# Kernel optimization log

Measured on AMD Instinct MI355X. Metric: run time of the kernel, lower is better.

The kernel has to match this reference:

```python
import jax, jax.numpy as jnp
import numpy as np

B, C, H, W = 4, 256, 128, 128
OUT = 50

def setup_inputs() -> dict:
    key = jax.random.key(0)
    k1, k2, k3 = jax.random.split(key, 3)
    x = jax.random.normal(k1, (B, C, H, W), dtype=jnp.float32)
    # conv2d 1x1 weights, kaiming-ish scale
    W_f = jax.random.normal(k2, (OUT, C), dtype=jnp.float32) * (1.0 / np.sqrt(C))
    W_beta = jax.random.normal(k3, (C, C), dtype=jnp.float32) * (1.0 / np.sqrt(C))
    return {"x": x, "W_f": W_f, "W_beta": W_beta}

def reference(x, W_f, W_beta):
    b, c, h, w = x.shape
    n = h * w
    xf = x.reshape(b, c, n)                      # [B,C,N]
    F = jnp.einsum('oc,bcn->bon', W_f, xf)       # 1x1 conv -> [B,O,N]
    # S = softmax(F @ A, axis over C), A = xf^T : [B,N,C]
    S = jnp.einsum('bon,bcn->boc', F, xf)        # [B,O,C]
    S = jax.nn.softmax(S, axis=2)
    St = jnp.swapaxes(S, 1, 2)                   # [B,C,O]
    E = jnp.einsum('bco,bon->bcn', St, F)        # [B,C,N]
    E = E.reshape(b, c, h, w)
    E = jnp.einsum('dc,bchw->bdhw', W_beta, E) + x  # beta conv + residual
    return E
```

## Files before the change

kernel.cpp:

```cpp
#include <hip/hip_runtime.h>
#include <math.h>

#define CCH 256
#define OCH 50
#define NPIX 16384
#define BATCH 4
#define BO (BATCH*OCH)
#define NSPLIT2 256
#define KC2 (NPIX/NSPLIT2)

typedef _Float16 f16x8 __attribute__((ext_vector_type(8)));
typedef float f32x4 __attribute__((ext_vector_type(4)));
typedef unsigned int uint;
typedef unsigned short ushort;

__device__ __forceinline__ void cvt_split(const float4 v0, const float4 v1,
                                          f16x8& h, f16x8& l) {
    float v[8] = {v0.x, v0.y, v0.z, v0.w, v1.x, v1.y, v1.z, v1.w};
#pragma unroll
    for (int j = 0; j < 8; ++j) {
        _Float16 hj = (_Float16)v[j];
        h[j] = hj;
        l[j] = (_Float16)(v[j] - (float)hj);
    }
}

__device__ __forceinline__ uint packhl(float v) {
    _Float16 h = (_Float16)v;
    _Float16 l = (_Float16)(v - (float)h);
    union { _Float16 f; ushort u; } H, L;
    H.f = h; L.f = l;
    return (uint)H.u | ((uint)L.u << 16);
}

__device__ __forceinline__ void unpack8(const uint* w, f16x8& h, f16x8& l) {
    union { uint u[4]; f16x8 v; } H, L;
#pragma unroll
    for (int k = 0; k < 4; ++k) {
        H.u[k] = __builtin_amdgcn_perm(w[2 * k + 1], w[2 * k], 0x05040100u);
        L.u[k] = __builtin_amdgcn_perm(w[2 * k + 1], w[2 * k], 0x07060302u);
    }
    h = H.v; l = L.v;
}

__global__ void k0_pack(const float* __restrict__ Wf, uint* __restrict__ Wf16p) {
    int i = blockIdx.x * 256 + threadIdx.x;
    if (i < 64 * CCH) {
        int o = i / CCH;
        float v = (o < OCH) ? Wf[i] : 0.f;
        Wf16p[i] = packhl(v);
    }
}

__global__ __launch_bounds__(256, 4) void k12_mfma(const float* __restrict__ x,
                                                   const uint* __restrict__ Wf16p,
                                                   float* __restrict__ F,
                                                   float* __restrict__ Spart) {
    int b  = blockIdx.y;
    int ks = blockIdx.x;
    int p0 = ks * KC2;
    int t  = threadIdx.x;
    int w = t >> 6, lane = t & 63, r16 = lane & 15, kg = lane >> 4;
    __shared__ uint xl[2][32 * 64];
    __shared__ float Ft[4][16 * 68];

    int cidx = t & 15;
    int pixg = t >> 4;
    const float* xb = x + ((size_t)b * CCH) * NPIX + p0;

    float4 r0 = *(const float4*)(xb + (size_t)cidx * NPIX + pixg * 4);
    float4 r1 = *(const float4*)(xb + (size_t)(16 + cidx) * NPIX + pixg * 4);

    f32x4 acc[4];
#pragma unroll
    for (int nt = 0; nt < 4; ++nt) acc[nt] = {0.f, 0.f, 0.f, 0.f};

    const uint* Arow = Wf16p + (w * 16 + r16) * CCH;

    {
        float v0[4] = {r0.x, r0.y, r0.z, r0.w};
        float v1[4] = {r1.x, r1.y, r1.z, r1.w};
#pragma unroll
        for (int j = 0; j < 4; ++j) {
            int pix = pixg * 4 + j;
            int q = (pix & 7) << 2;
            xl[0][pix * 32 + (cidx ^ q)]        = packhl(v0[j]);
            xl[0][pix * 32 + ((16 + cidx) ^ q)] = packhl(v1[j]);
        }
    }
    __syncthreads();

#pragma unroll
    for (int s = 0; s < 8; ++s) {
        if (s < 7) {
            r0 = *(const float4*)(xb + (size_t)((s + 1) * 32 + cidx) * NPIX + pixg * 4);
            r1 = *(const float4*)(xb + (size_t)((s + 1) * 32 + 16 + cidx) * NPIX + pixg * 4);
        }
        uint aw[8];
        *(uint4*)aw       = *(const uint4*)(Arow + s * 32 + kg * 8);
        *(uint4*)(aw + 4) = *(const uint4*)(Arow + s * 32 + kg * 8 + 4);
        f16x8 Ah, Al;
        unpack8(aw, Ah, Al);

        const uint* buf = xl[s & 1];
#pragma unroll
        for (int nt = 0; nt < 4; ++nt) {
            int pix = nt * 16 + r16;
            int q = (r16 & 7) << 2;
            uint bw[8];
            *(uint4*)bw       = *(const uint4*)&buf[pix * 32 + ((kg * 8) ^ q)];
            *(uint4*)(bw + 4) = *(const uint4*)&buf[pix * 32 + ((kg * 8 + 4) ^ q)];
            f16x8 Bh, Bl;
            unpack8(bw, Bh, Bl);
            acc[nt] = __builtin_amdgcn_mfma_f32_16x16x32_f16(Ah, Bh, acc[nt], 0, 0, 0);
            acc[nt] = __builtin_amdgcn_mfma_f32_16x16x32_f16(Ah, Bl, acc[nt], 0, 0, 0);
            acc[nt] = __builtin_amdgcn_mfma_f32_16x16x32_f16(Al, Bh, acc[nt], 0, 0, 0);
        }
        if (s < 7) {
            float v0[4] = {r0.x, r0.y, r0.z, r0.w};
            float v1[4] = {r1.x, r1.y, r1.z, r1.w};
            uint* nbuf = xl[(s + 1) & 1];
#pragma unroll
            for (int j = 0; j < 4; ++j) {
                int pix = pixg * 4 + j;
                int q = (pix & 7) << 2;
                nbuf[pix * 32 + (cidx ^ q)]        = packhl(v0[j]);
                nbuf[pix * 32 + ((16 + cidx) ^ q)] = packhl(v1[j]);
            }
            __syncthreads();
        }
    }

    float* Fb = F + ((size_t)b * 64 + w * 16 + kg * 4) * NPIX + p0;
#pragma unroll
    for (int nt = 0; nt < 4; ++nt)
#pragma unroll
        for (int r = 0; r < 4; ++r)
            Fb[(size_t)r * NPIX + nt * 16 + r16] = acc[nt][r];

    float* ft = Ft[w];
#pragma unroll
    for (int nt = 0; nt < 4; ++nt)
#pragma unroll
        for (int r = 0; r < 4; ++r)
            ft[(kg * 4 + r) * 68 + nt * 16 + r16] = acc[nt][r];
    __syncthreads();

    f16x8 Ah0, Al0, Ah1, Al1;
    {
        const float* fr = ft + r16 * 68;
        cvt_split(*(const float4*)(fr + kg * 8), *(const float4*)(fr + kg * 8 + 4), Ah0, Al0);
        cvt_split(*(const float4*)(fr + 32 + kg * 8), *(const float4*)(fr + 32 + kg * 8 + 4), Ah1, Al1);
    }

    const float* Bb = x + ((size_t)b * CCH) * NPIX + p0 + kg * 8;
#pragma unroll
    for (int half = 0; half < 2; ++half) {
        f32x4 sacc[8];
#pragma unroll
        for (int i = 0; i < 8; ++i) sacc[i] = {0.f, 0.f, 0.f, 0.f};
#pragma unroll
        for (int ct = 0; ct < 8; ++ct) {
            int c = (half * 8 + ct) * 16 + r16;
            const float* bp = Bb + (size_t)c * NPIX;
            f16x8 bh, bl;
            cvt_split(*(const float4*)bp, *(const float4*)(bp + 4), bh, bl);
            sacc[ct] = __builtin_amdgcn_mfma_f32_16x16x32_f16(Ah0, bh, sacc[ct], 0, 0, 0);
            sacc[ct] = __builtin_amdgcn_mfma_f32_16x16x32_f16(Ah0, bl, sacc[ct], 0, 0, 0);
            sacc[ct] = __builtin_amdgcn_mfma_f32_16x16x32_f16(Al0, bh, sacc[ct], 0, 0, 0);
            cvt_split(*(const float4*)(bp + 32), *(const float4*)(bp + 36), bh, bl);
            sacc[ct] = __builtin_amdgcn_mfma_f32_16x16x32_f16(Ah1, bh, sacc[ct], 0, 0, 0);
            sacc[ct] = __builtin_amdgcn_mfma_f32_16x16x32_f16(Ah1, bl, sacc[ct], 0, 0, 0);
            sacc[ct] = __builtin_amdgcn_mfma_f32_16x16x32_f16(Al1, bh, sacc[ct], 0, 0, 0);
        }
        float* Sp = Spart + (((size_t)ks * BATCH + b) * 64 + w * 16 + kg * 4) * 256
                  + half * 128 + r16;
#pragma unroll
        for (int ct = 0; ct < 8; ++ct)
#pragma unroll
            for (int r = 0; r < 4; ++r)
                Sp[(size_t)r * 256 + ct * 16] = sacc[ct][r];
    }
}

__global__ __launch_bounds__(1024) void k2r_softmax(const float* __restrict__ Spart,
                                                    float* __restrict__ S) {
    int row = blockIdx.x;
    int b = row / OCH, o = row % OCH;
    int tid = threadIdx.x;
    int c = tid & 255, g = tid >> 8;
    __shared__ float part[4][CCH];
    __shared__ float red[8];
    float v = 0.f;
    const size_t ksStride = (size_t)BATCH * 64 * 256;
    const float* p = Spart + ((size_t)(g * (NSPLIT2 / 4)) * BATCH + b) * 64 * 256
                   + (size_t)o * 256 + c;
#pragma unroll 8
    for (int ks = 0; ks < NSPLIT2 / 4; ++ks)
        v += p[ks * ksStride];
    part[g][c] = v;
    __syncthreads();
    float vv = 0.f, e = 0.f, m;
    if (tid < 256) {
        vv = part[0][c] + part[1][c] + part[2][c] + part[3][c];
        m = vv;
#pragma unroll
        for (int off = 32; off > 0; off >>= 1) m = fmaxf(m, __shfl_xor(m, off, 64));
        if ((tid & 63) == 0) red[tid >> 6] = m;
    }
    __syncthreads();
    if (tid < 256) {
        m = fmaxf(fmaxf(red[0], red[1]), fmaxf(red[2], red[3]));
        e = expf(vv - m);
        float s = e;
#pragma unroll
        for (int off = 32; off > 0; off >>= 1) s += __shfl_xor(s, off, 64);
        if ((tid & 63) == 0) red[4 + (tid >> 6)] = s;
    }
    __syncthreads();
    if (tid < 256) {
        float tot = red[4] + red[5] + red[6] + red[7];
        S[(size_t)row * CCH + c] = e / tot;
    }
}

__global__ __launch_bounds__(256) void k3_M(const float* __restrict__ Wbeta,
                                            const float* __restrict__ S,
                                            float* __restrict__ Mt) {
    int row = blockIdx.x;
    int d = threadIdx.x;
    const float* srow = S + (size_t)row * CCH;
    const float4* wb = (const float4*)(Wbeta + (size_t)d * CCH);
    float acc = 0.f;
#pragma unroll 4
    for (int cg = 0; cg < CCH / 4; ++cg) {
        float4 w = wb[cg];
        float4 s = *(const float4*)(srow + cg * 4);
        acc += w.x * s.x + w.y * s.y + w.z * s.z + w.w * s.w;
    }
    Mt[(size_t)row * CCH + d] = acc;
}

__global__ __launch_bounds__(256) void k4_out(const float* __restrict__ x,
                                              const float* __restrict__ F,
                                              const float* __restrict__ Mt,
                                              float* __restrict__ out) {
    int b  = blockIdx.z;
    int dq = blockIdx.y;
    int n  = blockIdx.x * 256 + threadIdx.x;
    float acc[32];
#pragma unroll
    for (int dd = 0; dd < 32; ++dd) acc[dd] = 0.f;
    const float* Fp = F + (size_t)b * 64 * NPIX + n;
    const float* mt = Mt + (size_t)b * OCH * CCH + dq * 32;
#pragma unroll 2
    for (int o = 0; o < OCH; ++o) {
        float fo = Fp[(size_t)o * NPIX];
        const float* m = mt + o * CCH;
#pragma unroll
        for (int dd = 0; dd < 32; ++dd) acc[dd] = fmaf(m[dd], fo, acc[dd]);
    }
    const float* xp = x + ((size_t)b * CCH + dq * 32) * NPIX + n;
    float* op = out + ((size_t)b * CCH + dq * 32) * NPIX + n;
#pragma unroll
    for (int dd = 0; dd < 32; ++dd)
        __builtin_nontemporal_store(acc[dd] + xp[(size_t)dd * NPIX], &op[(size_t)dd * NPIX]);
}

extern "C" void kernel_launch(void* const* d_in, const int* in_sizes, int n_in,
                              void* d_out, int out_size, void* d_ws, size_t ws_size,
                              hipStream_t stream) {
    const float* x     = (const float*)d_in[0];
    const float* Wf    = (const float*)d_in[1];
    const float* Wbeta = (const float*)d_in[2];
    float* out = (float*)d_out;

    float* F     = (float*)d_ws;
    uint*  Wf16p = (uint*)(F + (size_t)BATCH * 64 * NPIX);
    float* S     = (float*)(Wf16p + 64 * CCH);
    float* Mt    = S + (size_t)BO * CCH;
    float* Spart = out;

    k0_pack<<<dim3((64 * CCH + 255) / 256), dim3(256), 0, stream>>>(Wf, Wf16p);
    k12_mfma<<<dim3(NSPLIT2, BATCH), dim3(256), 0, stream>>>(x, Wf16p, F, Spart);
    k2r_softmax<<<dim3(BO), dim3(1024), 0, stream>>>(Spart, S);
    k3_M<<<dim3(BO), dim3(256), 0, stream>>>(Wbeta, S, Mt);
    k4_out<<<dim3(NPIX / 256, 8, BATCH), dim3(256), 0, stream>>>(x, F, Mt, out);
}
```

Baseline: 193.8 us.

## Fold W_f into per-batch CxC matrix and compute output via split-fp16 MFMA GEMM

Instead of storing F to global memory and re-reading it in the output kernel, the output is computed as out = G·x + x with G = Mt^T·W_f, a per-batch 256x256 matrix built by a new small kernel. The final stage becomes an MFMA GEMM over x using hi/lo fp16 splitting, which removes the F write and read traffic and the scalar FMA loop. In exchange it does more flops (K=256 instead of 50), adds an extra kernel launch, and keeps heavy register use for the 4x4 accumulator tiles.

```diff
diff --git a/kernel.cpp b/kernel.cpp
--- a/kernel.cpp
+++ b/kernel.cpp
@@ -54,7 +54,6 @@
 
 __global__ __launch_bounds__(256, 4) void k12_mfma(const float* __restrict__ x,
                                                    const uint* __restrict__ Wf16p,
-                                                   float* __restrict__ F,
                                                    float* __restrict__ Spart) {
     int b  = blockIdx.y;
     int ks = blockIdx.x;
@@ -130,13 +129,6 @@
             __syncthreads();
         }
     }
-
-    float* Fb = F + ((size_t)b * 64 + w * 16 + kg * 4) * NPIX + p0;
-#pragma unroll
-    for (int nt = 0; nt < 4; ++nt)
-#pragma unroll
-        for (int r = 0; r < 4; ++r)
-            Fb[(size_t)r * NPIX + nt * 16 + r16] = acc[nt][r];
 
     float* ft = Ft[w];
 #pragma unroll
@@ -241,30 +233,116 @@
     Mt[(size_t)row * CCH + d] = acc;
 }
 
-__global__ __launch_bounds__(256) void k4_out(const float* __restrict__ x,
-                                              const float* __restrict__ F,
-                                              const float* __restrict__ Mt,
-                                              float* __restrict__ out) {
-    int b  = blockIdx.z;
-    int dq = blockIdx.y;
-    int n  = blockIdx.x * 256 + threadIdx.x;
-    float acc[32];
-#pragma unroll
-    for (int dd = 0; dd < 32; ++dd) acc[dd] = 0.f;
-    const float* Fp = F + (size_t)b * 64 * NPIX + n;
-    const float* mt = Mt + (size_t)b * OCH * CCH + dq * 32;
-#pragma unroll 2
-    for (int o = 0; o < OCH; ++o) {
-        float fo = Fp[(size_t)o * NPIX];
-        const float* m = mt + o * CCH;
-#pragma unroll
-        for (int dd = 0; dd < 32; ++dd) acc[dd] = fmaf(m[dd], fo, acc[dd]);
-    }
-    const float* xp = x + ((size_t)b * CCH + dq * 32) * NPIX + n;
-    float* op = out + ((size_t)b * CCH + dq * 32) * NPIX + n;
-#pragma unroll
-    for (int dd = 0; dd < 32; ++dd)
-        __builtin_nontemporal_store(acc[dd] + xp[(size_t)dd * NPIX], &op[(size_t)dd * NPIX]);
+__global__ __launch_bounds__(256) void k3b_G(const float* __restrict__ Mt,
+                                             const float* __restrict__ Wf,
+                                             uint* __restrict__ Gp) {
+    int bd = blockIdx.x;
+    int b = bd >> 8, d = bd & 255;
+    int c = threadIdx.x;
+    float acc = 0.f;
+    const float* mp = Mt + ((size_t)b * OCH) * CCH + d;
+#pragma unroll 5
+    for (int o = 0; o < OCH; ++o)
+        acc = fmaf(mp[(size_t)o * CCH], Wf[o * CCH + c], acc);
+    Gp[(size_t)bd * CCH + c] = packhl(acc);
+}
+
+__global__ __launch_bounds__(256, 3) void k4_mfma(const float* __restrict__ x,
+                                                  const uint* __restrict__ Gp,
+                                                  float* __restrict__ out) {
+    int b  = blockIdx.y;
+    int ks = blockIdx.x;
+    int p0 = ks * KC2;
+    int t  = threadIdx.x;
+    int w = t >> 6, lane = t & 63, r16 = lane & 15, kg = lane >> 4;
+    __shared__ uint xl[2][32 * 64];
+
+    int cidx = t & 15;
+    int pixg = t >> 4;
+    const float* xb = x + ((size_t)b * CCH) * NPIX + p0;
+
+    float4 r0 = *(const float4*)(xb + (size_t)cidx * NPIX + pixg * 4);
+    float4 r1 = *(const float4*)(xb + (size_t)(16 + cidx) * NPIX + pixg * 4);
+
+    f32x4 acc[4][4];
+#pragma unroll
+    for (int mt = 0; mt < 4; ++mt)
+#pragma unroll
+        for (int nt = 0; nt < 4; ++nt) acc[mt][nt] = {0.f, 0.f, 0.f, 0.f};
+
+    const uint* Gb = Gp + ((size_t)b * 256 + w * 64 + r16) * CCH;
+
+    {
+        float v0[4] = {r0.x, r0.y, r0.z, r0.w};
+        float v1[4] = {r1.x, r1.y, r1.z, r1.w};
+#pragma unroll
+        for (int j = 0; j < 4; ++j) {
+            int pix = pixg * 4 + j;
+            int q = (pix & 7) << 2;
+            xl[0][pix * 32 + (cidx ^ q)]        = packhl(v0[j]);
+            xl[0][pix * 32 + ((16 + cidx) ^ q)] = packhl(v1[j]);
+        }
+    }
+    __syncthreads();
+
+#pragma unroll
+    for (int s = 0; s < 8; ++s) {
+        if (s < 7) {
+            r0 = *(const float4*)(xb + (size_t)((s + 1) * 32 + cidx) * NPIX + pixg * 4);
+            r1 = *(const float4*)(xb + (size_t)((s + 1) * 32 + 16 + cidx) * NPIX + pixg * 4);
+        }
+        f16x8 Bh[4], Bl[4];
+        const uint* buf = xl[s & 1];
+        int q = (r16 & 7) << 2;
+#pragma unroll
+        for (int nt = 0; nt < 4; ++nt) {
+            int pix = nt * 16 + r16;
+            uint bw[8];
+            *(uint4*)bw       = *(const uint4*)&buf[pix * 32 + ((kg * 8) ^ q)];
+            *(uint4*)(bw + 4) = *(const uint4*)&buf[pix * 32 + ((kg * 8 + 4) ^ q)];
+            unpack8(bw, Bh[nt], Bl[nt]);
+        }
+#pragma unroll
+        for (int mt = 0; mt < 4; ++mt) {
+            uint aw[8];
+            const uint* ap = Gb + (size_t)(mt * 16) * CCH + s * 32 + kg * 8;
+            *(uint4*)aw       = *(const uint4*)ap;
+            *(uint4*)(aw + 4) = *(const uint4*)(ap + 4);
+            f16x8 Ah, Al;
+            unpack8(aw, Ah, Al);
+#pragma unroll
+            for (int nt = 0; nt < 4; ++nt) {
+                acc[mt][nt] = __builtin_amdgcn_mfma_f32_16x16x32_f16(Ah, Bh[nt], acc[mt][nt], 0, 0, 0);
+                acc[mt][nt] = __builtin_amdgcn_mfma_f32_16x16x32_f16(Ah, Bl[nt], acc[mt][nt], 0, 0, 0);
+                acc[mt][nt] = __builtin_amdgcn_mfma_f32_16x16x32_f16(Al, Bh[nt], acc[mt][nt], 0, 0, 0);
+            }
+        }
+        if (s < 7) {
+            float v0[4] = {r0.x, r0.y, r0.z, r0.w};
+            float v1[4] = {r1.x, r1.y, r1.z, r1.w};
+            uint* nbuf = xl[(s + 1) & 1];
+#pragma unroll
+            for (int j = 0; j < 4; ++j) {
+                int pix = pixg * 4 + j;
+                int qq = (pix & 7) << 2;
+                nbuf[pix * 32 + (cidx ^ qq)]        = packhl(v0[j]);
+                nbuf[pix * 32 + ((16 + cidx) ^ qq)] = packhl(v1[j]);
+            }
+            __syncthreads();
+        }
+    }
+
+    const float* xr = x + ((size_t)b * CCH + w * 64 + kg * 4) * NPIX + p0 + r16;
+    float*       op = out + ((size_t)b * CCH + w * 64 + kg * 4) * NPIX + p0 + r16;
+#pragma unroll
+    for (int mt = 0; mt < 4; ++mt)
+#pragma unroll
+        for (int nt = 0; nt < 4; ++nt)
+#pragma unroll
+            for (int r = 0; r < 4; ++r) {
+                size_t o2 = (size_t)(mt * 16 + r) * NPIX + nt * 16;
+                __builtin_nontemporal_store(acc[mt][nt][r] + xr[o2], &op[o2]);
+            }
 }
 
 extern "C" void kernel_launch(void* const* d_in, const int* in_sizes, int n_in,
@@ -275,15 +353,16 @@
     const float* Wbeta = (const float*)d_in[2];
     float* out = (float*)d_out;
 
-    float* F     = (float*)d_ws;
-    uint*  Wf16p = (uint*)(F + (size_t)BATCH * 64 * NPIX);
+    uint*  Wf16p = (uint*)d_ws;
     float* S     = (float*)(Wf16p + 64 * CCH);
     float* Mt    = S + (size_t)BO * CCH;
+    uint*  Gp    = (uint*)(Mt + (size_t)BO * CCH);
     float* Spart = out;
 
     k0_pack<<<dim3((64 * CCH + 255) / 256), dim3(256), 0, stream>>>(Wf, Wf16p);
-    k12_mfma<<<dim3(NSPLIT2, BATCH), dim3(256), 0, stream>>>(x, Wf16p, F, Spart);
+    k12_mfma<<<dim3(NSPLIT2, BATCH), dim3(256), 0, stream>>>(x, Wf16p, Spart);
     k2r_softmax<<<dim3(BO), dim3(1024), 0, stream>>>(Spart, S);
     k3_M<<<dim3(BO), dim3(256), 0, stream>>>(Wbeta, S, Mt);
-    k4_out<<<dim3(NPIX / 256, 8, BATCH), dim3(256), 0, stream>>>(x, F, Mt, out);
-}
+    k3b_G<<<dim3(BATCH * 256), dim3(256), 0, stream>>>(Mt, Wf, Gp);
+    k4_mfma<<<dim3(NSPLIT2, BATCH), dim3(256), 0, stream>>>(x, Gp, out);
+}
```

New measurement: 219.6 us. +13.3%, slower.

## Fold W_beta·S·W_f into per-batch matrix and compute output with split-fp16 MFMA

Applied to the files above, without the earlier changes.

The final stage is reformulated algebraically: G = Mt^T·W_f + I is precomputed per batch, so out = G·x runs as a split-fp16 MFMA GEMM over a transposed fp16 hi/lo copy of x. This removes the write and reread of F and folds the residual into the identity term. A new pre-pass transposes x into pixel-major hi/lo planes, which both MFMA kernels read directly instead of converting through LDS. The cost is an extra full pass over x plus a large fp16 workspace, and the 256x256 K=256 GEMM does more FLOPs than the rank-50 path.

```diff
diff --git a/kernel.cpp b/kernel.cpp
--- a/kernel.cpp
+++ b/kernel.cpp
@@ -33,110 +33,83 @@
     return (uint)H.u | ((uint)L.u << 16);
 }
 
-__device__ __forceinline__ void unpack8(const uint* w, f16x8& h, f16x8& l) {
-    union { uint u[4]; f16x8 v; } H, L;
-#pragma unroll
-    for (int k = 0; k < 4; ++k) {
-        H.u[k] = __builtin_amdgcn_perm(w[2 * k + 1], w[2 * k], 0x05040100u);
-        L.u[k] = __builtin_amdgcn_perm(w[2 * k + 1], w[2 * k], 0x07060302u);
-    }
-    h = H.v; l = L.v;
-}
-
-__global__ void k0_pack(const float* __restrict__ Wf, uint* __restrict__ Wf16p) {
+__global__ void k0_split(const float* __restrict__ Wf, _Float16* __restrict__ Wfh,
+                         _Float16* __restrict__ Wfl) {
     int i = blockIdx.x * 256 + threadIdx.x;
-    if (i < 64 * CCH) {
-        int o = i / CCH;
-        float v = (o < OCH) ? Wf[i] : 0.f;
-        Wf16p[i] = packhl(v);
-    }
+    int o = i >> 8;
+    float v = (o < OCH) ? Wf[i] : 0.f;
+    _Float16 h = (_Float16)v;
+    Wfh[i] = h;
+    Wfl[i] = (_Float16)(v - (float)h);
+}
+
+__global__ __launch_bounds__(256) void kT_split(const float* __restrict__ x,
+                                                _Float16* __restrict__ xTh,
+                                                _Float16* __restrict__ xTl) {
+    int b = blockIdx.z, c0 = blockIdx.y * 64, p0 = blockIdx.x * 64;
+    __shared__ uint tl[64 * 65];
+    int t = threadIdx.x;
+    int cr = t >> 2, pq = t & 3;
+    const float* xp = x + ((size_t)(b * CCH + c0 + cr)) * NPIX + p0 + pq * 16;
+#pragma unroll
+    for (int g = 0; g < 4; ++g) {
+        float4 v = *(const float4*)(xp + g * 4);
+        float vv[4] = {v.x, v.y, v.z, v.w};
+#pragma unroll
+        for (int j = 0; j < 4; ++j)
+            tl[cr * 65 + pq * 16 + g * 4 + j] = packhl(vv[j]);
+    }
+    __syncthreads();
+    int pr = t >> 2, cq = t & 3;
+    union { ushort u[16]; uint4 q[2]; } H, L;
+#pragma unroll
+    for (int j = 0; j < 16; ++j) {
+        uint u = tl[(cq * 16 + j) * 65 + pr];
+        H.u[j] = (ushort)(u & 0xffff);
+        L.u[j] = (ushort)(u >> 16);
+    }
+    size_t ob = ((size_t)b * NPIX + p0 + pr) * CCH + c0 + cq * 16;
+    *(uint4*)(xTh + ob)     = H.q[0];
+    *(uint4*)(xTh + ob + 8) = H.q[1];
+    *(uint4*)(xTl + ob)     = L.q[0];
+    *(uint4*)(xTl + ob + 8) = L.q[1];
 }
 
 __global__ __launch_bounds__(256, 4) void k12_mfma(const float* __restrict__ x,
-                                                   const uint* __restrict__ Wf16p,
-                                                   float* __restrict__ F,
+                                                   const _Float16* __restrict__ Wfh,
+                                                   const _Float16* __restrict__ Wfl,
+                                                   const _Float16* __restrict__ xTh,
+                                                   const _Float16* __restrict__ xTl,
                                                    float* __restrict__ Spart) {
     int b  = blockIdx.y;
     int ks = blockIdx.x;
     int p0 = ks * KC2;
     int t  = threadIdx.x;
     int w = t >> 6, lane = t & 63, r16 = lane & 15, kg = lane >> 4;
-    __shared__ uint xl[2][32 * 64];
     __shared__ float Ft[4][16 * 68];
 
-    int cidx = t & 15;
-    int pixg = t >> 4;
-    const float* xb = x + ((size_t)b * CCH) * NPIX + p0;
-
-    float4 r0 = *(const float4*)(xb + (size_t)cidx * NPIX + pixg * 4);
-    float4 r1 = *(const float4*)(xb + (size_t)(16 + cidx) * NPIX + pixg * 4);
-
     f32x4 acc[4];
 #pragma unroll
     for (int nt = 0; nt < 4; ++nt) acc[nt] = {0.f, 0.f, 0.f, 0.f};
 
-    const uint* Arow = Wf16p + (w * 16 + r16) * CCH;
-
-    {
-        float v0[4] = {r0.x, r0.y, r0.z, r0.w};
-        float v1[4] = {r1.x, r1.y, r1.z, r1.w};
-#pragma unroll
-        for (int j = 0; j < 4; ++j) {
-            int pix = pixg * 4 + j;
-            int q = (pix & 7) << 2;
-            xl[0][pix * 32 + (cidx ^ q)]        = packhl(v0[j]);
-            xl[0][pix * 32 + ((16 + cidx) ^ q)] = packhl(v1[j]);
-        }
-    }
-    __syncthreads();
+    const _Float16* Ahp = Wfh + (w * 16 + r16) * CCH + kg * 8;
+    const _Float16* Alp = Wfl + (w * 16 + r16) * CCH + kg * 8;
+    const _Float16* Bhp = xTh + ((size_t)b * NPIX + p0 + r16) * CCH + kg * 8;
+    const _Float16* Blp = xTl + ((size_t)b * NPIX + p0 + r16) * CCH + kg * 8;
 
 #pragma unroll
     for (int s = 0; s < 8; ++s) {
-        if (s < 7) {
-            r0 = *(const float4*)(xb + (size_t)((s + 1) * 32 + cidx) * NPIX + pixg * 4);
-            r1 = *(const float4*)(xb + (size_t)((s + 1) * 32 + 16 + cidx) * NPIX + pixg * 4);
-        }
-        uint aw[8];
-        *(uint4*)aw       = *(const uint4*)(Arow + s * 32 + kg * 8);
-        *(uint4*)(aw + 4) = *(const uint4*)(Arow + s * 32 + kg * 8 + 4);
-        f16x8 Ah, Al;
-        unpack8(aw, Ah, Al);
-
-        const uint* buf = xl[s & 1];
+        f16x8 Ah = *(const f16x8*)(Ahp + s * 32);
+        f16x8 Al = *(const f16x8*)(Alp + s * 32);
 #pragma unroll
         for (int nt = 0; nt < 4; ++nt) {
-            int pix = nt * 16 + r16;
-            int q = (r16 & 7) << 2;
-            uint bw[8];
-            *(uint4*)bw       = *(const uint4*)&buf[pix * 32 + ((kg * 8) ^ q)];
-            *(uint4*)(bw + 4) = *(const uint4*)&buf[pix * 32 + ((kg * 8 + 4) ^ q)];
-            f16x8 Bh, Bl;
-            unpack8(bw, Bh, Bl);
+            f16x8 Bh = *(const f16x8*)(Bhp + (size_t)(nt * 16) * CCH + s * 32);
+            f16x8 Bl = *(const f16x8*)(Blp + (size_t)(nt * 16) * CCH + s * 32);
             acc[nt] = __builtin_amdgcn_mfma_f32_16x16x32_f16(Ah, Bh, acc[nt], 0, 0, 0);
             acc[nt] = __builtin_amdgcn_mfma_f32_16x16x32_f16(Ah, Bl, acc[nt], 0, 0, 0);
             acc[nt] = __builtin_amdgcn_mfma_f32_16x16x32_f16(Al, Bh, acc[nt], 0, 0, 0);
         }
-        if (s < 7) {
-            float v0[4] = {r0.x, r0.y, r0.z, r0.w};
-            float v1[4] = {r1.x, r1.y, r1.z, r1.w};
-            uint* nbuf = xl[(s + 1) & 1];
-#pragma unroll
-            for (int j = 0; j < 4; ++j) {
-                int pix = pixg * 4 + j;
-                int q = (pix & 7) << 2;
-                nbuf[pix * 32 + (cidx ^ q)]        = packhl(v0[j]);
-                nbuf[pix * 32 + ((16 + cidx) ^ q)] = packhl(v1[j]);
-            }
-            __syncthreads();
-        }
-    }
-
-    float* Fb = F + ((size_t)b * 64 + w * 16 + kg * 4) * NPIX + p0;
-#pragma unroll
-    for (int nt = 0; nt < 4; ++nt)
-#pragma unroll
-        for (int r = 0; r < 4; ++r)
-            Fb[(size_t)r * NPIX + nt * 16 + r16] = acc[nt][r];
+    }
 
     float* ft = Ft[w];
 #pragma unroll
@@ -241,30 +214,77 @@
     Mt[(size_t)row * CCH + d] = acc;
 }
 
-__global__ __launch_bounds__(256) void k4_out(const float* __restrict__ x,
-                                              const float* __restrict__ F,
-                                              const float* __restrict__ Mt,
-                                              float* __restrict__ out) {
-    int b  = blockIdx.z;
-    int dq = blockIdx.y;
-    int n  = blockIdx.x * 256 + threadIdx.x;
-    float acc[32];
-#pragma unroll
-    for (int dd = 0; dd < 32; ++dd) acc[dd] = 0.f;
-    const float* Fp = F + (size_t)b * 64 * NPIX + n;
-    const float* mt = Mt + (size_t)b * OCH * CCH + dq * 32;
-#pragma unroll 2
-    for (int o = 0; o < OCH; ++o) {
-        float fo = Fp[(size_t)o * NPIX];
-        const float* m = mt + o * CCH;
-#pragma unroll
-        for (int dd = 0; dd < 32; ++dd) acc[dd] = fmaf(m[dd], fo, acc[dd]);
-    }
-    const float* xp = x + ((size_t)b * CCH + dq * 32) * NPIX + n;
-    float* op = out + ((size_t)b * CCH + dq * 32) * NPIX + n;
-#pragma unroll
-    for (int dd = 0; dd < 32; ++dd)
-        __builtin_nontemporal_store(acc[dd] + xp[(size_t)dd * NPIX], &op[(size_t)dd * NPIX]);
+__global__ __launch_bounds__(256) void k3b_G(const float* __restrict__ Mt,
+                                             const float* __restrict__ Wf,
+                                             _Float16* __restrict__ Gh,
+                                             _Float16* __restrict__ Gl) {
+    int bd = blockIdx.x;
+    int b = bd >> 8, d = bd & 255;
+    int c = threadIdx.x;
+    float acc = (d == c) ? 1.f : 0.f;
+    const float* mp = Mt + ((size_t)b * OCH) * CCH + d;
+#pragma unroll 5
+    for (int o = 0; o < OCH; ++o)
+        acc = fmaf(mp[(size_t)o * CCH], Wf[o * CCH + c], acc);
+    _Float16 h = (_Float16)acc;
+    Gh[(size_t)bd * CCH + c] = h;
+    Gl[(size_t)bd * CCH + c] = (_Float16)(acc - (float)h);
+}
+
+__global__ __launch_bounds__(256, 3) void k4_mfma(const _Float16* __restrict__ xTh,
+                                                  const _Float16* __restrict__ xTl,
+                                                  const _Float16* __restrict__ Gh,
+                                                  const _Float16* __restrict__ Gl,
+                                                  float* __restrict__ out) {
+    int b  = blockIdx.y;
+    int ks = blockIdx.x;
+    int p0 = ks * KC2;
+    int t  = threadIdx.x;
+    int w = t >> 6, lane = t & 63, r16 = lane & 15, kg = lane >> 4;
+
+    f32x4 acc[4][4];
+#pragma unroll
+    for (int mt = 0; mt < 4; ++mt)
+#pragma unroll
+        for (int nt = 0; nt < 4; ++nt) acc[mt][nt] = {0.f, 0.f, 0.f, 0.f};
+
+    const _Float16* GhB = Gh + ((size_t)b * 256 + w * 64 + r16) * CCH + kg * 8;
+    const _Float16* GlB = Gl + ((size_t)b * 256 + w * 64 + r16) * CCH + kg * 8;
+    const _Float16* BhB = xTh + ((size_t)b * NPIX + p0 + r16) * CCH + kg * 8;
+    const _Float16* BlB = xTl + ((size_t)b * NPIX + p0 + r16) * CCH + kg * 8;
+
+#pragma unroll
+    for (int s = 0; s < 8; ++s) {
+        f16x8 Ah[4], Al[4], Bh[4], Bl[4];
+#pragma unroll
+        for (int mt = 0; mt < 4; ++mt) {
+            Ah[mt] = *(const f16x8*)(GhB + (size_t)(mt * 16) * CCH + s * 32);
+            Al[mt] = *(const f16x8*)(GlB + (size_t)(mt * 16) * CCH + s * 32);
+        }
+#pragma unroll
+        for (int nt = 0; nt < 4; ++nt) {
+            Bh[nt] = *(const f16x8*)(BhB + (size_t)(nt * 16) * CCH + s * 32);
+            Bl[nt] = *(const f16x8*)(BlB + (size_t)(nt * 16) * CCH + s * 32);
+        }
+#pragma unroll
+        for (int mt = 0; mt < 4; ++mt)
+#pragma unroll
+            for (int nt = 0; nt < 4; ++nt) {
+                acc[mt][nt] = __builtin_amdgcn_mfma_f32_16x16x32_f16(Ah[mt], Bh[nt], acc[mt][nt], 0, 0, 0);
+                acc[mt][nt] = __builtin_amdgcn_mfma_f32_16x16x32_f16(Ah[mt], Bl[nt], acc[mt][nt], 0, 0, 0);
+                acc[mt][nt] = __builtin_amdgcn_mfma_f32_16x16x32_f16(Al[mt], Bh[nt], acc[mt][nt], 0, 0, 0);
+            }
+    }
+
+    float* op = out + ((size_t)b * CCH + w * 64 + kg * 4) * NPIX + p0 + r16;
+#pragma unroll
+    for (int mt = 0; mt < 4; ++mt)
+#pragma unroll
+        for (int nt = 0; nt < 4; ++nt)
+#pragma unroll
+            for (int r = 0; r < 4; ++r)
+                __builtin_nontemporal_store(acc[mt][nt][r],
+                                            &op[(size_t)(mt * 16 + r) * NPIX + nt * 16]);
 }
 
 extern "C" void kernel_launch(void* const* d_in, const int* in_sizes, int n_in,
@@ -275,15 +295,22 @@
     const float* Wbeta = (const float*)d_in[2];
     float* out = (float*)d_out;
 
-    float* F     = (float*)d_ws;
-    uint*  Wf16p = (uint*)(F + (size_t)BATCH * 64 * NPIX);
-    float* S     = (float*)(Wf16p + 64 * CCH);
-    float* Mt    = S + (size_t)BO * CCH;
+    const size_t PLANE = (size_t)BATCH * NPIX * CCH;
+    _Float16* xTh = (_Float16*)d_ws;
+    _Float16* xTl = xTh + PLANE;
+    _Float16* Wfh = xTl + PLANE;
+    _Float16* Wfl = Wfh + 64 * CCH;
+    float*    S   = (float*)(Wfl + 64 * CCH);
+    float*    Mt  = S + (size_t)BO * CCH;
+    _Float16* Gh  = (_Float16*)(Mt + (size_t)BO * CCH);
+    _Float16* Gl  = Gh + (size_t)BATCH * 256 * CCH;
     float* Spart = out;
 
-    k0_pack<<<dim3((64 * CCH + 255) / 256), dim3(256), 0, stream>>>(Wf, Wf16p);
-    k12_mfma<<<dim3(NSPLIT2, BATCH), dim3(256), 0, stream>>>(x, Wf16p, F, Spart);
+    k0_split<<<dim3(64), dim3(256), 0, stream>>>(Wf, Wfh, Wfl);
+    kT_split<<<dim3(NPIX / 64, CCH / 64, BATCH), dim3(256), 0, stream>>>(x, xTh, xTl);
+    k12_mfma<<<dim3(NSPLIT2, BATCH), dim3(256), 0, stream>>>(x, Wfh, Wfl, xTh, xTl, Spart);
     k2r_softmax<<<dim3(BO), dim3(1024), 0, stream>>>(Spart, S);
     k3_M<<<dim3(BO), dim3(256), 0, stream>>>(Wbeta, S, Mt);
-    k4_out<<<dim3(NPIX / 256, 8, BATCH), dim3(256), 0, stream>>>(x, F, Mt, out);
-}
+    k3b_G<<<dim3(BATCH * 256), dim3(256), 0, stream>>>(Mt, Wf, Gh, Gl);
+    k4_mfma<<<dim3(NSPLIT2, BATCH), dim3(256), 0, stream>>>(xTh, xTl, Gh, Gl, out);
+}
```

After: 277.9 us. 43.4% more time.
